# Kernel optimization log

Measured on AMD Instinct MI355X. Metric: run time of the kernel, lower is better.

## Reference

```python
import jax, jax.numpy as jnp
import numpy as np

N_ATOMS = 768
BOX_L = 30.0
CUTOFF = 5.0


def _cp(a, b, c):
    # numpy equivalent of torch.cartesian_prod for 1-D inputs
    g = np.meshgrid(a, b, c, indexing='ij')
    return np.stack(g, axis=-1).reshape(-1, 3)


def get_shifts_np(box, pbc, cutoff):
    # host-side mirror of TorchNeighborList._get_shifts (data-dependent shapes)
    recip = np.linalg.inv(box).T
    inv_len = np.linalg.norm(recip, axis=1)
    nrep = np.where(pbc, np.ceil(cutoff * inv_len).astype(np.int64), 0)
    r1 = np.arange(1, nrep[0] + 1)
    r2 = np.arange(1, nrep[1] + 1)
    r3 = np.arange(1, nrep[2] + 1)
    o = np.zeros(1, dtype=np.int64)
    blocks = [_cp(r1, r2, r3), _cp(r1, r2, o), _cp(r1, r2, -r3),
              _cp(r1, o, r3), _cp(r1, o, o), _cp(r1, o, -r3),
              _cp(r1, -r2, r3), _cp(r1, -r2, o), _cp(r1, -r2, -r3),
              _cp(o, r2, r3), _cp(o, r2, o), _cp(o, r2, -r3), _cp(o, o, r3)]
    return np.concatenate(blocks, axis=0).astype(np.int32)


def setup_inputs() -> dict:
    key = jax.random.key(0)
    positions = jax.random.uniform(key, (N_ATOMS, 3), dtype=jnp.float32) * BOX_L
    box = jnp.eye(3, dtype=jnp.float32) * BOX_L
    shifts = jnp.asarray(get_shifts_np(np.eye(3) * BOX_L, np.array([True, True, True]), CUTOFF))  # (13, 3)
    return {"positions": positions, "box": box, "shifts": shifts, "cutoff": CUTOFF}


def reference(positions, box, shifts, cutoff):
    N = positions.shape[0]
    S = shifts.shape[0]
    # central-cell unique pairs i<j (torch.combinations)
    iu, ju = jnp.triu_indices(N, k=1)
    # shifted candidates: cartesian_prod(shift_index, i, j)
    shift_idx = jnp.repeat(jnp.arange(S), N * N)
    pi_s = jnp.tile(jnp.repeat(jnp.arange(N), N), S)
    pj_s = jnp.tile(jnp.arange(N), S * N)
    pi_all = jnp.concatenate([iu, pi_s])          # (P,)
    pj_all = jnp.concatenate([ju, pj_s])          # (P,)
    shifts_all = jnp.concatenate([jnp.zeros((iu.shape[0], 3), dtype=shifts.dtype), shifts[shift_idx]])  # (P,3)
    shift_vals = shifts_all.astype(box.dtype) @ box
    Rij = positions[pi_all] - positions[pj_all] + shift_vals  # (P,3)
    d = jnp.linalg.norm(Rij, axis=1)
    mask = d < cutoff
    # bidirectional pairs (torch.cat of (i,j) and (j,i)), offsets negated for the first half
    bi_i = jnp.concatenate([pi_all, pj_all])
    bi_j = jnp.concatenate([pj_all, pi_all])
    bi_off = jnp.concatenate([-shifts_all, shifts_all])
    bi_mask = jnp.concatenate([mask, mask])
    # jit-compatible compaction: sort by idx_i with invalid entries pushed to the end
    sort_key = jnp.where(bi_mask, bi_i, N)
    order = jnp.argsort(sort_key)  # jax sort is stable
    valid = bi_mask[order]
    idx_i = jnp.where(valid, bi_i[order], -1)
    idx_j = jnp.where(valid, bi_j[order], -1)
    offset = (bi_off[order].astype(box.dtype) @ box) * valid[:, None].astype(box.dtype)
    return idx_i, idx_j, offset, valid
```

## Files before the change

kernel.cpp:

```cpp
#include <hip/hip_runtime.h>

#pragma clang fp contract(off)


#define MAX_SHIFTS 64
#define FILL_ITERS 16

typedef float f32x4 __attribute__((ext_vector_type(4)));

__device__ __forceinline__ bool pv_fwd(float fx, float fy, float fz,
                                       const float* __restrict__ pos, int j,
                                       float sx, float sy, float sz, float cutoff) {
  float dx = fx - pos[j * 3 + 0] + sx;
  float dy = fy - pos[j * 3 + 1] + sy;
  float dz = fz - pos[j * 3 + 2] + sz;
  float d2 = dx * dx + dy * dy + dz * dz;
  return sqrtf(d2) < cutoff;
}

__device__ __forceinline__ bool pv_bwd(const float* __restrict__ pos, int a,
                                       float fx, float fy, float fz,
                                       float sx, float sy, float sz, float cutoff) {
  float dx = pos[a * 3 + 0] - fx + sx;
  float dy = pos[a * 3 + 1] - fy + sy;
  float dz = pos[a * 3 + 2] - fz + sz;
  float d2 = dx * dx + dy * dy + dz * dz;
  return sqrtf(d2) < cutoff;
}

__device__ __forceinline__ void load_shift_vecs(const float* __restrict__ box,
                                                const int* __restrict__ shifts,
                                                int S, float* sv, int tid, int nthreads) {
  for (int s = tid; s < S; s += nthreads) {
    float s0 = (float)shifts[s * 3 + 0];
    float s1 = (float)shifts[s * 3 + 1];
    float s2 = (float)shifts[s * 3 + 2];
    sv[s * 3 + 0] = s0 * box[0] + s1 * box[3] + s2 * box[6];
    sv[s * 3 + 1] = s0 * box[1] + s1 * box[4] + s2 * box[7];
    sv[s * 3 + 2] = s0 * box[2] + s1 * box[5] + s2 * box[8];
  }
}

__device__ __forceinline__ bool axis_ok(float lo, float hi, float cutpad) {
  return (hi > -cutpad) && (lo < cutpad);
}

__global__ __launch_bounds__(256) void k_count(
    const float* __restrict__ pos, const float* __restrict__ box,
    const int* __restrict__ shifts, const float* __restrict__ cutp,
    int N, int S, int* __restrict__ count) {
  __shared__ float sv[MAX_SHIFTS * 3];
  __shared__ float bred[4][6];
  __shared__ int rf[4], rb[4];
  int atom = blockIdx.x;
  int t = threadIdx.x;
  float cut = cutp[0];
  float cutpad = cut + fmaxf(cut * 1e-5f, 1e-5f);
  load_shift_vecs(box, shifts, S, sv, t, blockDim.x);

  float mnx = 1e30f, mny = 1e30f, mnz = 1e30f, mxx = -1e30f, mxy = -1e30f, mxz = -1e30f;
  for (int i = t; i < N; i += blockDim.x) {
    float x = pos[3 * i + 0], y = pos[3 * i + 1], z = pos[3 * i + 2];
    mnx = fminf(mnx, x); mny = fminf(mny, y); mnz = fminf(mnz, z);
    mxx = fmaxf(mxx, x); mxy = fmaxf(mxy, y); mxz = fmaxf(mxz, z);
  }
  for (int off = 32; off; off >>= 1) {
    mnx = fminf(mnx, __shfl_xor(mnx, off)); mny = fminf(mny, __shfl_xor(mny, off));
    mnz = fminf(mnz, __shfl_xor(mnz, off)); mxx = fmaxf(mxx, __shfl_xor(mxx, off));
    mxy = fmaxf(mxy, __shfl_xor(mxy, off)); mxz = fmaxf(mxz, __shfl_xor(mxz, off));
  }
  int w = t >> 6;
  if ((t & 63) == 0) {
    bred[w][0] = mnx; bred[w][1] = mny; bred[w][2] = mnz;
    bred[w][3] = mxx; bred[w][4] = mxy; bred[w][5] = mxz;
  }
  __syncthreads();
  int nw = blockDim.x >> 6;
  mnx = bred[0][0]; mny = bred[0][1]; mnz = bred[0][2];
  mxx = bred[0][3]; mxy = bred[0][4]; mxz = bred[0][5];
  for (int ww = 1; ww < nw; ww++) {
    mnx = fminf(mnx, bred[ww][0]); mny = fminf(mny, bred[ww][1]); mnz = fminf(mnz, bred[ww][2]);
    mxx = fmaxf(mxx, bred[ww][3]); mxy = fmaxf(mxy, bred[ww][4]); mxz = fmaxf(mxz, bred[ww][5]);
  }

  float pix = pos[3 * atom + 0], piy = pos[3 * atom + 1], piz = pos[3 * atom + 2];
  int cf = 0, cb = 0;
  for (int j = atom + 1 + t; j < N; j += blockDim.x)
    if (pv_fwd(pix, piy, piz, pos, j, 0.f, 0.f, 0.f, cut)) cf++;
  for (int a = t; a < atom; a += blockDim.x)
    if (pv_bwd(pos, a, pix, piy, piz, 0.f, 0.f, 0.f, cut)) cb++;

  for (int s = 0; s < S; s++) {
    float svx = sv[3 * s + 0], svy = sv[3 * s + 1], svz = sv[3 * s + 2];
    bool af = axis_ok((pix - mxx) + svx, (pix - mnx) + svx, cutpad) &&
              axis_ok((piy - mxy) + svy, (piy - mny) + svy, cutpad) &&
              axis_ok((piz - mxz) + svz, (piz - mnz) + svz, cutpad);
    if (af) {
      for (int j = t; j < N; j += blockDim.x)
        if (pv_fwd(pix, piy, piz, pos, j, svx, svy, svz, cut)) cf++;
    }
    bool ab = axis_ok((mnx - pix) + svx, (mxx - pix) + svx, cutpad) &&
              axis_ok((mny - piy) + svy, (mxy - piy) + svy, cutpad) &&
              axis_ok((mnz - piz) + svz, (mxz - piz) + svz, cutpad);
    if (ab) {
      for (int a = t; a < N; a += blockDim.x)
        if (pv_bwd(pos, a, pix, piy, piz, svx, svy, svz, cut)) cb++;
    }
  }
  for (int off = 32; off; off >>= 1) {
    cf += __shfl_down(cf, off);
    cb += __shfl_down(cb, off);
  }
  if ((t & 63) == 0) { rf[w] = cf; rb[w] = cb; }
  __syncthreads();
  if (t == 0) {
    int f = 0, b = 0;
    for (int ww = 0; ww < nw; ww++) { f += rf[ww]; b += rb[ww]; }
    count[2 * atom + 0] = f;
    count[2 * atom + 1] = b;
  }
}

__global__ __launch_bounds__(256) void k_scan(const int* __restrict__ count,
                                              int* __restrict__ start, int n2) {
  __shared__ int part[256];
  int t = threadIdx.x;
  int chunk = (n2 + 255) >> 8;
  int lo = t * chunk;
  int hi = min(lo + chunk, n2);
  int s = 0;
  for (int i = lo; i < hi; i++) s += count[i];
  part[t] = s;
  __syncthreads();
  for (int off = 1; off < 256; off <<= 1) {
    int v = (t >= off) ? part[t - off] : 0;
    __syncthreads();
    part[t] += v;
    __syncthreads();
  }
  int run = part[t] - s;
  for (int i = lo; i < hi; i++) { start[i] = run; run += count[i]; }
  if (t == 255) start[n2] = part[255];
}

__global__ __launch_bounds__(256) void k_main(
    const float* __restrict__ pos, const float* __restrict__ box,
    const int* __restrict__ shifts, const float* __restrict__ cutp,
    int N, int S, const int* __restrict__ start,
    float* __restrict__ out, long M, long n4, int NWB) {
  __shared__ float sv[MAX_SHIFTS * 3];
  int t = threadIdx.x;

  if ((int)blockIdx.x < NWB) {
    float cut = cutp[0];
    float cutpad = cut + fmaxf(cut * 1e-5f, 1e-5f);
    load_shift_vecs(box, shifts, S, sv, t, 256);
    __syncthreads();
    int w = t >> 6, lane = t & 63;
    int g = blockIdx.x * 4 + w;
    if (g >= 2 * N) return;
    int atom = g >> 1;
    int dir = g & 1;

    float mnx = 1e30f, mny = 1e30f, mnz = 1e30f, mxx = -1e30f, mxy = -1e30f, mxz = -1e30f;
    for (int i = lane; i < N; i += 64) {
      float x = pos[3 * i + 0], y = pos[3 * i + 1], z = pos[3 * i + 2];
      mnx = fminf(mnx, x); mny = fminf(mny, y); mnz = fminf(mnz, z);
      mxx = fmaxf(mxx, x); mxy = fmaxf(mxy, y); mxz = fmaxf(mxz, z);
    }
    for (int off = 32; off; off >>= 1) {
      mnx = fminf(mnx, __shfl_xor(mnx, off)); mny = fminf(mny, __shfl_xor(mny, off));
      mnz = fminf(mnz, __shfl_xor(mnz, off)); mxx = fmaxf(mxx, __shfl_xor(mxx, off));
      mxy = fmaxf(mxy, __shfl_xor(mxy, off)); mxz = fmaxf(mxz, __shfl_xor(mxz, off));
    }

    long base = start[g];
    float* __restrict__ out_i = out;
    float* __restrict__ out_j = out + M;
    float* __restrict__ out_off = out + 2 * M;
    float* __restrict__ out_v = out + 5 * M;

    float pix = pos[3 * atom + 0], piy = pos[3 * atom + 1], piz = pos[3 * atom + 2];
    float fatom = (float)atom;
    int running = 0;

    {
      int n = (dir == 0) ? (N - 1 - atom) : atom;
      int j0 = (dir == 0) ? (atom + 1) : 0;
      float oz0 = (dir == 0) ? -0.0f : 0.0f;
      for (int c0 = 0; c0 < n; c0 += 64) {
        int c = c0 + lane;
        bool v = false;
        int other = j0 + c;
        if (c < n) {
          v = (dir == 0) ? pv_fwd(pix, piy, piz, pos, other, 0.f, 0.f, 0.f, cut)
                         : pv_bwd(pos, other, pix, piy, piz, 0.f, 0.f, 0.f, cut);
        }
        unsigned long long m = __ballot(v);
        if (v) {
          int rank = __popcll(m & ((1ULL << lane) - 1ULL));
          long row = base + running + rank;
          out_i[row] = fatom;
          out_j[row] = (float)other;
          out_off[row * 3 + 0] = oz0;
          out_off[row * 3 + 1] = oz0;
          out_off[row * 3 + 2] = oz0;
          out_v[row] = 1.0f;
        }
        running += __popcll(m);
      }
    }
    for (int s = 0; s < S; s++) {
      float svx = sv[3 * s + 0], svy = sv[3 * s + 1], svz = sv[3 * s + 2];
      bool active;
      if (dir == 0) {
        active = axis_ok((pix - mxx) + svx, (pix - mnx) + svx, cutpad) &&
                 axis_ok((piy - mxy) + svy, (piy - mny) + svy, cutpad) &&
                 axis_ok((piz - mxz) + svz, (piz - mnz) + svz, cutpad);
      } else {
        active = axis_ok((mnx - pix) + svx, (mxx - pix) + svx, cutpad) &&
                 axis_ok((mny - piy) + svy, (mxy - piy) + svy, cutpad) &&
                 axis_ok((mnz - piz) + svz, (mxz - piz) + svz, cutpad);
      }
      if (!active) continue;
      float ox = (dir == 0) ? -svx : svx;
      float oy = (dir == 0) ? -svy : svy;
      float oz = (dir == 0) ? -svz : svz;
      for (int c0 = 0; c0 < N; c0 += 64) {
        int other = c0 + lane;
        bool v = false;
        if (other < N) {
          v = (dir == 0) ? pv_fwd(pix, piy, piz, pos, other, svx, svy, svz, cut)
                         : pv_bwd(pos, other, pix, piy, piz, svx, svy, svz, cut);
        }
        unsigned long long m = __ballot(v);
        if (v) {
          int rank = __popcll(m & ((1ULL << lane) - 1ULL));
          long row = base + running + rank;
          out_i[row] = fatom;
          out_j[row] = (float)other;
          out_off[row * 3 + 0] = ox;
          out_off[row * 3 + 1] = oy;
          out_off[row * 3 + 2] = oz;
          out_v[row] = 1.0f;
        }
        running += __popcll(m);
      }
    }
  } else {
    long fb = (long)blockIdx.x - NWB;
    long kbase = fb * (256L * FILL_ITERS);
    long total = (long)start[2 * N];
    long E0 = total;
    long E1 = M + total;
    long E2 = 2 * M + 3 * total;
    long E3 = 5 * M + total;
    const f32x4 neg = {-1.f, -1.f, -1.f, -1.f};
    const f32x4 zer = {0.f, 0.f, 0.f, 0.f};
    f32x4* __restrict__ out4 = (f32x4*)out;
    for (int it = 0; it < FILL_ITERS; it++) {
      long k = kbase + (long)it * 256 + t;
      if (k >= n4) break;
      long e = k << 2;
      long ve = (e < M) ? E0 : ((e < 2 * M) ? E1 : ((e < 5 * M) ? E2 : E3));
      if (e + 4 <= ve) continue;
      bool isneg = (e < 2 * M);
      if (e >= ve) {
        __builtin_nontemporal_store(isneg ? neg : zer, &out4[k]);
      } else {
        float dv = isneg ? -1.f : 0.f;
        for (int q = 0; q < 4; q++)
          if (e + q >= ve) out[e + q] = dv;
      }
    }
  }
}

extern "C" void kernel_launch(void* const* d_in, const int* in_sizes, int n_in,
                              void* d_out, int out_size, void* d_ws, size_t ws_size,
                              hipStream_t stream) {
  const float* pos = (const float*)d_in[0];
  const float* box = (const float*)d_in[1];
  const int* shifts = (const int*)d_in[2];
  const float* cutp = (const float*)d_in[3];
  int N = in_sizes[0] / 3;
  int S = in_sizes[2] / 3;
  long M = (long)out_size / 6;
  float* out = (float*)d_out;

  int* count = (int*)d_ws;
  int* start = count + 2 * N;

  long n4 = (long)out_size / 4;
  int NWB = (2 * N + 3) / 4;
  int NFB = (int)((n4 + (256L * FILL_ITERS) - 1) / (256L * FILL_ITERS));

  hipLaunchKernelGGL(k_count, dim3(N), dim3(256), 0, stream,
                     pos, box, shifts, cutp, N, S, count);
  hipLaunchKernelGGL(k_scan, dim3(1), dim3(256), 0, stream, count, start, 2 * N);
  hipLaunchKernelGGL(k_main, dim3(NWB + NFB), dim3(256), 0, stream,
                     pos, box, shifts, cutp, N, S, start, out, M, n4, NWB);
}
```

Before: 102.9 us.

## Drop the scan kernel and compute prefix offsets redundantly in the main kernel

```diff
diff --git a/kernel.cpp b/kernel.cpp
--- a/kernel.cpp
+++ b/kernel.cpp
@@ -121,44 +121,23 @@
   }
 }
 
-__global__ __launch_bounds__(256) void k_scan(const int* __restrict__ count,
-                                              int* __restrict__ start, int n2) {
-  __shared__ int part[256];
-  int t = threadIdx.x;
-  int chunk = (n2 + 255) >> 8;
-  int lo = t * chunk;
-  int hi = min(lo + chunk, n2);
-  int s = 0;
-  for (int i = lo; i < hi; i++) s += count[i];
-  part[t] = s;
-  __syncthreads();
-  for (int off = 1; off < 256; off <<= 1) {
-    int v = (t >= off) ? part[t - off] : 0;
-    __syncthreads();
-    part[t] += v;
-    __syncthreads();
-  }
-  int run = part[t] - s;
-  for (int i = lo; i < hi; i++) { start[i] = run; run += count[i]; }
-  if (t == 255) start[n2] = part[255];
-}
-
 __global__ __launch_bounds__(256) void k_main(
     const float* __restrict__ pos, const float* __restrict__ box,
     const int* __restrict__ shifts, const float* __restrict__ cutp,
-    int N, int S, const int* __restrict__ start,
+    int N, int S, const int* __restrict__ count,
     float* __restrict__ out, long M, long n4, int NWB) {
   __shared__ float sv[MAX_SHIFTS * 3];
   int t = threadIdx.x;
+  int lane = t & 63, w = t >> 6;
+  int n2 = 2 * N;
 
   if ((int)blockIdx.x < NWB) {
     float cut = cutp[0];
     float cutpad = cut + fmaxf(cut * 1e-5f, 1e-5f);
     load_shift_vecs(box, shifts, S, sv, t, 256);
     __syncthreads();
-    int w = t >> 6, lane = t & 63;
     int g = blockIdx.x * 4 + w;
-    if (g >= 2 * N) return;
+    if (g >= n2) return;
     int atom = g >> 1;
     int dir = g & 1;
 
@@ -174,7 +153,11 @@
       mxy = fmaxf(mxy, __shfl_xor(mxy, off)); mxz = fmaxf(mxz, __shfl_xor(mxz, off));
     }
 
-    long base = start[g];
+    int pre = 0;
+    for (int i = lane; i < g; i += 64) pre += count[i];
+    for (int off = 32; off; off >>= 1) pre += __shfl_xor(pre, off);
+    long base = pre;
+
     float* __restrict__ out_i = out;
     float* __restrict__ out_j = out + M;
     float* __restrict__ out_off = out + 2 * M;
@@ -248,9 +231,17 @@
       }
     }
   } else {
+    int tot = 0;
+    for (int i = lane; i < n2; i += 64) tot += count[i];
+    for (int off = 32; off; off >>= 1) tot += __shfl_xor(tot, off);
+    long total = tot;
+
     long fb = (long)blockIdx.x - NWB;
-    long kbase = fb * (256L * FILL_ITERS);
-    long total = (long)start[2 * N];
+    long k_lo = fb * (256L * FILL_ITERS);
+    long k_hi = k_lo + 256L * FILL_ITERS;
+    if (k_hi > n4) k_hi = n4;
+    long e_lo = k_lo << 2, e_hi = k_hi << 2;
+
     long E0 = total;
     long E1 = M + total;
     long E2 = 2 * M + 3 * total;
@@ -258,19 +249,32 @@
     const f32x4 neg = {-1.f, -1.f, -1.f, -1.f};
     const f32x4 zer = {0.f, 0.f, 0.f, 0.f};
     f32x4* __restrict__ out4 = (f32x4*)out;
-    for (int it = 0; it < FILL_ITERS; it++) {
-      long k = kbase + (long)it * 256 + t;
-      if (k >= n4) break;
-      long e = k << 2;
-      long ve = (e < M) ? E0 : ((e < 2 * M) ? E1 : ((e < 5 * M) ? E2 : E3));
-      if (e + 4 <= ve) continue;
-      bool isneg = (e < 2 * M);
-      if (e >= ve) {
-        __builtin_nontemporal_store(isneg ? neg : zer, &out4[k]);
-      } else {
-        float dv = isneg ? -1.f : 0.f;
-        for (int q = 0; q < 4; q++)
-          if (e + q >= ve) out[e + q] = dv;
+
+    int s0 = (e_lo < M) ? 0 : ((e_lo < 2 * M) ? 1 : ((e_lo < 5 * M) ? 2 : 3));
+    long eh = e_hi - 1;
+    int s1 = (eh < M) ? 0 : ((eh < 2 * M) ? 1 : ((eh < 5 * M) ? 2 : 3));
+    long ve0 = (s0 == 0) ? E0 : ((s0 == 1) ? E1 : ((s0 == 2) ? E2 : E3));
+
+    if ((k_hi - k_lo) == 256L * FILL_ITERS && s0 == s1 && e_lo >= ve0) {
+      f32x4 val = (s0 < 2) ? neg : zer;
+      f32x4* __restrict__ p = out4 + k_lo + t;
+#pragma unroll
+      for (int it = 0; it < FILL_ITERS; it++) p[(long)it * 256] = val;
+    } else {
+      for (int it = 0; it < FILL_ITERS; it++) {
+        long k = k_lo + (long)it * 256 + t;
+        if (k >= n4) break;
+        long e = k << 2;
+        long ve = (e < M) ? E0 : ((e < 2 * M) ? E1 : ((e < 5 * M) ? E2 : E3));
+        if (e + 4 <= ve) continue;
+        bool isneg = (e < 2 * M);
+        if (e >= ve) {
+          out4[k] = isneg ? neg : zer;
+        } else {
+          float dv = isneg ? -1.f : 0.f;
+          for (int q = 0; q < 4; q++)
+            if (e + q >= ve) out[e + q] = dv;
+        }
       }
     }
   }
@@ -289,7 +293,6 @@
   float* out = (float*)d_out;
 
   int* count = (int*)d_ws;
-  int* start = count + 2 * N;
 
   long n4 = (long)out_size / 4;
   int NWB = (2 * N + 3) / 4;
@@ -297,7 +300,6 @@
 
   hipLaunchKernelGGL(k_count, dim3(N), dim3(256), 0, stream,
                      pos, box, shifts, cutp, N, S, count);
-  hipLaunchKernelGGL(k_scan, dim3(1), dim3(256), 0, stream, count, start, 2 * N);
   hipLaunchKernelGGL(k_main, dim3(NWB + NFB), dim3(256), 0, stream,
-                     pos, box, shifts, cutp, N, S, start, out, M, n4, NWB);
-}
+                     pos, box, shifts, cutp, N, S, count, out, M, n4, NWB);
+}
```

Result: faster. 94.28 us (-8.4%).
